# Optimization experiments

Hardware: AMD Instinct MI355X
Metric: run time of the kernel (lower is better)

Reference implementation:

```python
import jax, jax.numpy as jnp
import numpy as np

BS, C_IN, H, W = 16, 128, 64, 64
C_OUT, K, STRIDE, PAD, DIL = 256, 3, 1, 1, 1
ALPHA = 0.5  # scaling_factor
QMAX = 127.0  # int8 symmetric fake-quant


def _fake_quant(t):
    # symmetric per-tensor int8 fake quantization with straight-through estimator
    s = jax.lax.stop_gradient(jnp.max(jnp.abs(t))) / QMAX
    s = jnp.where(s == 0, 1.0, s)
    q = jnp.clip(jnp.round(t / s), -QMAX, QMAX) * s
    return t + jax.lax.stop_gradient(q - t)  # STE


def setup_inputs() -> dict:
    key = jax.random.key(0)
    k1, k2, k3 = jax.random.split(key, 3)
    x = jax.random.normal(k1, (BS, C_IN, H, W), dtype=jnp.float32)
    weight = jax.random.normal(k2, (C_OUT, C_IN, K, K), dtype=jnp.float32) * 0.05
    bias = jax.random.normal(k3, (C_OUT,), dtype=jnp.float32) * 0.01
    return {"x": x, "weight": weight, "bias": bias}


def reference(x, weight, bias):
    bs, _, h_in, w_in = x.shape
    ickhkw = C_IN * K * K
    h_out = (h_in + 2 * PAD - DIL * (K - 1) - 1) // STRIDE + 1
    w_out = (w_in + 2 * PAD - DIL * (K - 1) - 1) // STRIDE + 1

    # im2col (matches torch F.unfold feature ordering: channel-major, then kh, kw)
    patches = jax.lax.conv_general_dilated_patches(
        x, filter_shape=(K, K), window_strides=(STRIDE, STRIDE),
        padding=((PAD, PAD), (PAD, PAD)), rhs_dilation=(DIL, DIL),
    )  # [bs, ickhkw, h_out, w_out]
    cols = patches.reshape(bs, ickhkw, h_out * w_out)
    cols = cols.transpose(0, 2, 1).reshape(-1, ickhkw)  # [bs*L, ickhkw]

    w2 = weight.reshape(C_OUT, ickhkw)

    # SmoothQuant per-column scales (detached)
    w_scale = jax.lax.stop_gradient(jnp.max(jnp.abs(w2), axis=0))    # [ickhkw]
    act_scale = jax.lax.stop_gradient(jnp.max(jnp.abs(cols), axis=0))  # [ickhkw]
    scale = act_scale ** ALPHA / w_scale ** (1.0 - ALPHA)
    scale = jnp.where(scale == 0, 1.0, scale)

    w_s = _fake_quant(w2 * scale)
    x_s = _fake_quant(cols / scale)

    out = x_s @ w_s.T  # [bs*L, C_OUT]
    out = out.reshape(bs, h_out * w_out, C_OUT).transpose(0, 2, 1)
    out = out.reshape(bs, C_OUT, h_out, w_out)
    return out + bias.reshape(1, C_OUT, 1, 1)
```

## Files before the change

### kernel.cpp

```cpp
#include <hip/hip_runtime.h>
#include <cstdint>

#define C_IN   128
#define C_OUT  256
#define KK     1152
#define NPIX   4096
#define BS     16
#define M_ROWS 65536
#define QMAXF  127.0f

typedef int v4i __attribute__((ext_vector_type(4)));

#define OFF_QW    75497472
#define OFF_SCALE 75792384
#define OFF_QMUL  75796992
#define OFF_APART 75801600
#define OFF_SCAL  75843072

__global__ void k_prep(const float* __restrict__ x, const float* __restrict__ wgt,
                       float* __restrict__ act_part, float* __restrict__ w_part) {
    const int tid = threadIdx.x;
    if (blockIdx.x >= 1024) {
        int t = blockIdx.x - 1024;
        int j = (t % 5) * 256 + tid;
        int s = t / 5;
        if (j >= KK) return;
        const float* p = wgt + (size_t)s * 16 * KK + j;
        float m = 0.f;
#pragma unroll
        for (int i = 0; i < 16; i++) m = fmaxf(m, fabsf(p[(size_t)i * KK]));
        w_part[s * KK + j] = m;
        return;
    }
    const int c = blockIdx.x >> 3, s = blockIdx.x & 7;
    float m[9];
#pragma unroll
    for (int i = 0; i < 9; i++) m[i] = 0.f;
    for (int p = tid; p < 2 * NPIX; p += 256) {
        int b = s * 2 + (p >> 12);
        int hw = p & 4095;
        int h = hw >> 6, w = hw & 63;
        float v = fabsf(x[b * (C_IN * NPIX) + c * NPIX + hw]);
        bool rr[3] = { h <= 62, true, h >= 1 };
        bool cc[3] = { w <= 62, true, w >= 1 };
#pragma unroll
        for (int i = 0; i < 3; i++)
#pragma unroll
            for (int jq = 0; jq < 3; jq++)
                m[i * 3 + jq] = fmaxf(m[i * 3 + jq], (rr[i] && cc[jq]) ? v : 0.f);
    }
    __shared__ float sm[9][4];
    int lane = tid & 63, wid = tid >> 6;
#pragma unroll
    for (int i = 0; i < 9; i++) {
        float v = m[i];
        for (int off = 32; off > 0; off >>= 1) v = fmaxf(v, __shfl_down(v, off));
        if (lane == 0) sm[i][wid] = v;
    }
    __syncthreads();
    if (tid < 9) {
        float v = fmaxf(fmaxf(sm[tid][0], sm[tid][1]), fmaxf(sm[tid][2], sm[tid][3]));
        act_part[s * KK + c * 9 + tid] = v;
    }
}

__global__ void k_scales(const float* __restrict__ act_part, const float* __restrict__ w_part,
                         float* __restrict__ scale, float* __restrict__ qmul,
                         float* __restrict__ scalars) {
    const int tid = threadIdx.x;
    float sc_local[2] = {1.f, 1.f};
    float mx = 0.f, mw = 0.f;
#pragma unroll
    for (int t = 0; t < 2; t++) {
        int j = tid + t * 1024;
        if (j < KK) {
            float a = 0.f;
#pragma unroll
            for (int s = 0; s < 8; s++) a = fmaxf(a, act_part[s * KK + j]);
            float wv = 0.f;
#pragma unroll
            for (int s = 0; s < 16; s++) wv = fmaxf(wv, w_part[s * KK + j]);
            float sc = sqrtf(a) / sqrtf(wv);
            if (sc == 0.f) sc = 1.0f;
            scale[j] = sc;
            sc_local[t] = sc;
            mx = fmaxf(mx, a / sc);
            mw = fmaxf(mw, wv * sc);
        }
    }
    __shared__ float smx[16], smw[16];
    __shared__ float s_x_sh;
    int lane = tid & 63, wid = tid >> 6;
    for (int off = 32; off > 0; off >>= 1) {
        mx = fmaxf(mx, __shfl_down(mx, off));
        mw = fmaxf(mw, __shfl_down(mw, off));
    }
    if (lane == 0) { smx[wid] = mx; smw[wid] = mw; }
    __syncthreads();
    if (tid == 0) {
        float a = 0.f, b = 0.f;
        for (int i = 0; i < 16; i++) { a = fmaxf(a, smx[i]); b = fmaxf(b, smw[i]); }
        float s_x = a / QMAXF; if (s_x == 0.f) s_x = 1.f;
        float s_w = b / QMAXF; if (s_w == 0.f) s_w = 1.f;
        scalars[0] = s_x; scalars[1] = s_w; scalars[2] = s_x * s_w;
        s_x_sh = s_x;
    }
    __syncthreads();
    float s_x = s_x_sh;
#pragma unroll
    for (int t = 0; t < 2; t++) {
        int j = tid + t * 1024;
        if (j < KK) qmul[j] = 1.0f / (sc_local[t] * s_x);
    }
}

__global__ void k_quant_w(const float* __restrict__ wgt, const float* __restrict__ scale,
                          const float* __restrict__ scalars, signed char* __restrict__ qWp) {
    int idx = blockIdx.x * 256 + threadIdx.x;
    int m  = (unsigned)idx / KK;
    int kp = idx - m * KK;
    int tap = kp >> 7, c = kp & 127;
    int j = c * 9 + tap;
    float s_w = scalars[1];
    float t = wgt[m * KK + j] * scale[j];
    float q = rintf(t / s_w);
    q = fminf(fmaxf(q, -QMAXF), QMAXF);
    qWp[idx] = (signed char)(int)q;
}

#define PRODUCE(TP, XV, BSP)                                                    \
    do {                                                                        \
        const int g_ = (TP) / 3, jj_ = (TP) - g_ * 3, sh_ = jj_ - 1;            \
        const bool rowok_ = ((unsigned)(oh - 1 + g_)) < 64u;                    \
        int n_ = lane - sh_;                                                    \
        bool valid_ = (unsigned)n_ < 64u;                                       \
        int wrow_ = valid_ ? n_ : (sh_ == -1 ? 0 : 63);                         \
        bool live_ = rowok_ && valid_;                                          \
        const float* qmt_ = qm + (TP) * 128 + c0;                               \
        int pk_[4];                                                             \
        _Pragma("unroll")                                                       \
        for (int d4 = 0; d4 < 4; d4++) {                                        \
            int w_ = 0;                                                         \
            _Pragma("unroll")                                                   \
            for (int e = 0; e < 4; e++) {                                       \
                float v_ = live_ ? XV[d4 * 4 + e] : 0.f;                        \
                float q_ = rintf(v_ * qmt_[d4 * 4 + e]);                        \
                q_ = fminf(fmaxf(q_, -QMAXF), QMAXF);                           \
                w_ |= ((int)q_ & 255) << (8 * e);                               \
            }                                                                   \
            pk_[d4] = w_;                                                       \
        }                                                                       \
        *(v4i*)((BSP) + wrow_ * 128 + ((wv ^ (wrow_ & 7)) * 16)) =              \
            (v4i){pk_[0], pk_[1], pk_[2], pk_[3]};                              \
    } while (0)

__global__ __launch_bounds__(512, 4) void k_gemm(const signed char* __restrict__ qWp,
                                                 const float* __restrict__ x,
                                                 const float* __restrict__ qmul,
                                                 const float* __restrict__ scalars,
                                                 const float* __restrict__ bias,
                                                 float* __restrict__ out) {
    __shared__ __align__(16) signed char Bs[2][64 * 128];
    __shared__ float qm[KK];
    const int tid = threadIdx.x;
    const int lane = tid & 63, wv = tid >> 6;
    const int b  = blockIdx.x >> 6;
    const int oh = blockIdx.x & 63;
    const float* xb = x + (size_t)b * (C_IN * NPIX);
    const int c0 = wv * 16;

    for (int i = tid; i < KK; i += 512) {
        int tap = i >> 7, c = i & 127;
        qm[i] = qmul[c * 9 + tap];
    }

    const signed char* aBase = qWp + (size_t)(wv * 32 + (lane & 15)) * KK + (lane >> 4) * 16;

    v4i acc[2][4];
#pragma unroll
    for (int i = 0; i < 2; i++)
#pragma unroll
        for (int jq = 0; jq < 4; jq++) acc[i][jq] = (v4i){0, 0, 0, 0};

    float xr[16], xrn[16];
    {
        const bool ok = oh >= 1;
        const float* s = xb + (oh - 1) * 64 + lane;
#pragma unroll
        for (int d = 0; d < 16; d++) xr[d] = ok ? s[(size_t)(c0 + d) * NPIX] : 0.f;
    }
    v4i af[2][2], afn[2][2];
#pragma unroll
    for (int h = 0; h < 2; h++)
#pragma unroll
        for (int mt = 0; mt < 2; mt++)
            af[h][mt] = *(const v4i*)(aBase + (size_t)mt * 16 * KK + 0 * 128 + h * 64);

    __syncthreads();

    PRODUCE(0, xr, (signed char*)Bs[0]);

    {
        const float* sp = xb + oh * 64 + lane;
#pragma unroll
        for (int d = 0; d < 16; d++) xrn[d] = sp[(size_t)(c0 + d) * NPIX];
    }

    __syncthreads();

#pragma unroll
    for (int t = 0; t < 9; t++) {
        const signed char* bsR = (const signed char*)Bs[t & 1];
        signed char* bsW = (signed char*)Bs[(t + 1) & 1];

        v4i bf0[4];
#pragma unroll
        for (int nt = 0; nt < 4; nt++) {
            int rb = nt * 16 + (lane & 15);
            int q4 = (lane >> 4);
            bf0[nt] = *(const v4i*)(bsR + rb * 128 + ((q4 ^ (rb & 7)) * 16));
        }

        if (t < 8) {
#pragma unroll
            for (int h = 0; h < 2; h++)
#pragma unroll
                for (int mt = 0; mt < 2; mt++)
                    afn[h][mt] = *(const v4i*)(aBase + (size_t)mt * 16 * KK + (t + 1) * 128 + h * 64);
        }

        if (t == 2) {
            const bool ok = (oh + 1) < 64;
            const float* sp = xb + (oh + 1) * 64 + lane;
#pragma unroll
            for (int d = 0; d < 16; d++) xr[d] = ok ? sp[(size_t)(c0 + d) * NPIX] : 0.f;
        }

        if (t < 8) {
            const int tap = t + 1;
            const int g = tap / 3;
            if (g == 1) PRODUCE(tap, xrn, bsW);
            else        PRODUCE(tap, xr,  bsW);
        }

#pragma unroll
        for (int mt = 0; mt < 2; mt++)
#pragma unroll
            for (int nt = 0; nt < 4; nt++)
                acc[mt][nt] = __builtin_amdgcn_mfma_i32_16x16x64_i8(af[0][mt], bf0[nt], acc[mt][nt], 0, 0, 0);

        v4i bf1[4];
#pragma unroll
        for (int nt = 0; nt < 4; nt++) {
            int rb = nt * 16 + (lane & 15);
            int q4 = 4 + (lane >> 4);
            bf1[nt] = *(const v4i*)(bsR + rb * 128 + ((q4 ^ (rb & 7)) * 16));
        }
#pragma unroll
        for (int mt = 0; mt < 2; mt++)
#pragma unroll
            for (int nt = 0; nt < 4; nt++)
                acc[mt][nt] = __builtin_amdgcn_mfma_i32_16x16x64_i8(af[1][mt], bf1[nt], acc[mt][nt], 0, 0, 0);

        if (t < 8) {
#pragma unroll
            for (int h = 0; h < 2; h++)
#pragma unroll
                for (int mt = 0; mt < 2; mt++) af[h][mt] = afn[h][mt];
            __syncthreads();
        }
    }

    const float ssp = scalars[2];
    const int quad = lane >> 4, col = lane & 15;
    float bv[2][4];
#pragma unroll
    for (int mt = 0; mt < 2; mt++)
#pragma unroll
        for (int rg = 0; rg < 4; rg++)
            bv[mt][rg] = bias[wv * 32 + mt * 16 + quad * 4 + rg];

    float* obase = out + ((size_t)b * C_OUT) * NPIX + oh * 64;
#pragma unroll
    for (int mt = 0; mt < 2; mt++) {
#pragma unroll
        for (int nt = 0; nt < 4; nt++) {
            int n = nt * 16 + col;
#pragma unroll
            for (int rg = 0; rg < 4; rg++) {
                int m = wv * 32 + mt * 16 + quad * 4 + rg;
                obase[(size_t)m * NPIX + n] = (float)acc[mt][nt][rg] * ssp + bv[mt][rg];
            }
        }
    }
}

extern "C" void kernel_launch(void* const* d_in, const int* in_sizes, int n_in,
                              void* d_out, int out_size, void* d_ws, size_t ws_size,
                              hipStream_t stream) {
    const float* x    = (const float*)d_in[0];
    const float* wgt  = (const float*)d_in[1];
    const float* bias = (const float*)d_in[2];
    float* out = (float*)d_out;

    char* ws = (char*)d_ws;
    signed char* qWp = (signed char*)(ws + OFF_QW);
    float* w_part    = (float*)(ws + OFF_QW);
    float* scale     = (float*)(ws + OFF_SCALE);
    float* qmul      = (float*)(ws + OFF_QMUL);
    float* act_part  = (float*)(ws + OFF_APART);
    float* scalars   = (float*)(ws + OFF_SCAL);

    k_prep<<<1104, 256, 0, stream>>>(x, wgt, act_part, w_part);
    k_scales<<<1, 1024, 0, stream>>>(act_part, w_part, scale, qmul, scalars);
    k_quant_w<<<(C_OUT * KK) / 256, 256, 0, stream>>>(wgt, scale, scalars, qWp);
    k_gemm<<<BS * 64, 512, 0, stream>>>(qWp, x, qmul, scalars, bias, out);
}
```

Baseline: 171.9 us.

## Batch three taps per LDS stage and streamline int8 packing in conv GEMM

The per-tap double-buffered loop is replaced by stages that each produce three taps (one input row) into a larger shared buffer. This cuts block barriers from nine to three and lets MFMA work on one row overlap the quantisation of the next. Quantisation packing now uses byte-permute instructions instead of clamp, shift and or, relying on the scales keeping values inside the int8 range and on out-of-range rows already being zero. Blocks are also remapped for better cache locality. The tripled LDS footprint may reduce how many blocks fit per CU.

New measurement: 156.4 us. 9.0% less time.

```diff
diff --git a/kernel.cpp b/kernel.cpp
--- a/kernel.cpp
+++ b/kernel.cpp
@@ -130,28 +130,59 @@
 
 #define PRODUCE(TP, XV, BSP)                                                    \
     do {                                                                        \
-        const int g_ = (TP) / 3, jj_ = (TP) - g_ * 3, sh_ = jj_ - 1;            \
-        const bool rowok_ = ((unsigned)(oh - 1 + g_)) < 64u;                    \
+        const int jj_ = (TP) % 3, sh_ = jj_ - 1;                                \
         int n_ = lane - sh_;                                                    \
         bool valid_ = (unsigned)n_ < 64u;                                       \
         int wrow_ = valid_ ? n_ : (sh_ == -1 ? 0 : 63);                         \
-        bool live_ = rowok_ && valid_;                                          \
         const float* qmt_ = qm + (TP) * 128 + c0;                               \
         int pk_[4];                                                             \
         _Pragma("unroll")                                                       \
         for (int d4 = 0; d4 < 4; d4++) {                                        \
-            int w_ = 0;                                                         \
-            _Pragma("unroll")                                                   \
-            for (int e = 0; e < 4; e++) {                                       \
-                float v_ = live_ ? XV[d4 * 4 + e] : 0.f;                        \
-                float q_ = rintf(v_ * qmt_[d4 * 4 + e]);                        \
-                q_ = fminf(fmaxf(q_, -QMAXF), QMAXF);                           \
-                w_ |= ((int)q_ & 255) << (8 * e);                               \
-            }                                                                   \
-            pk_[d4] = w_;                                                       \
+            int q0_ = (int)rintf(XV[d4 * 4 + 0] * qmt_[d4 * 4 + 0]);            \
+            int q1_ = (int)rintf(XV[d4 * 4 + 1] * qmt_[d4 * 4 + 1]);            \
+            int q2_ = (int)rintf(XV[d4 * 4 + 2] * qmt_[d4 * 4 + 2]);            \
+            int q3_ = (int)rintf(XV[d4 * 4 + 3] * qmt_[d4 * 4 + 3]);            \
+            unsigned t0_ = __builtin_amdgcn_perm((unsigned)q1_, (unsigned)q0_, 0x0c0c0400u); \
+            unsigned t1_ = __builtin_amdgcn_perm((unsigned)q3_, (unsigned)q2_, 0x0c0c0400u); \
+            int w_ = (int)__builtin_amdgcn_perm(t1_, t0_, 0x05040100u);         \
+            pk_[d4] = valid_ ? w_ : 0;                                          \
         }                                                                       \
         *(v4i*)((BSP) + wrow_ * 128 + ((wv ^ (wrow_ & 7)) * 16)) =              \
             (v4i){pk_[0], pk_[1], pk_[2], pk_[3]};                              \
+    } while (0)
+
+#define MFMA_TAP(TP, BSP)                                                       \
+    do {                                                                        \
+        if ((TP) < 8) {                                                         \
+            _Pragma("unroll")                                                   \
+            for (int h = 0; h < 2; h++)                                         \
+                _Pragma("unroll")                                               \
+                for (int mt = 0; mt < 2; mt++)                                  \
+                    afn[h][mt] = *(const v4i*)(aBase + (size_t)mt * 16 * KK +   \
+                                               ((TP) + 1) * 128 + h * 64);      \
+        }                                                                       \
+        _Pragma("unroll")                                                       \
+        for (int h = 0; h < 2; h++) {                                           \
+            const int q4_ = h * 4 + (lane >> 4);                                \
+            v4i bf_[4];                                                         \
+            _Pragma("unroll")                                                   \
+            for (int nt = 0; nt < 4; nt++) {                                    \
+                int rb_ = nt * 16 + (lane & 15);                                \
+                bf_[nt] = *(const v4i*)((BSP) + rb_ * 128 + ((q4_ ^ (rb_ & 7)) * 16)); \
+            }                                                                   \
+            _Pragma("unroll")                                                   \
+            for (int mt = 0; mt < 2; mt++)                                      \
+                _Pragma("unroll")                                               \
+                for (int nt = 0; nt < 4; nt++)                                  \
+                    acc[mt][nt] = __builtin_amdgcn_mfma_i32_16x16x64_i8(        \
+                        af[h][mt], bf_[nt], acc[mt][nt], 0, 0, 0);              \
+        }                                                                       \
+        if ((TP) < 8) {                                                         \
+            _Pragma("unroll")                                                   \
+            for (int h = 0; h < 2; h++)                                         \
+                _Pragma("unroll")                                               \
+                for (int mt = 0; mt < 2; mt++) af[h][mt] = afn[h][mt];          \
+        }                                                                       \
     } while (0)
 
 __global__ __launch_bounds__(512, 4) void k_gemm(const signed char* __restrict__ qWp,
@@ -160,12 +191,14 @@
                                                  const float* __restrict__ scalars,
                                                  const float* __restrict__ bias,
                                                  float* __restrict__ out) {
-    __shared__ __align__(16) signed char Bs[2][64 * 128];
+    __shared__ __align__(16) signed char Bs[2][3][64 * 128];
     __shared__ float qm[KK];
     const int tid = threadIdx.x;
     const int lane = tid & 63, wv = tid >> 6;
-    const int b  = blockIdx.x >> 6;
-    const int oh = blockIdx.x & 63;
+    const int bid = blockIdx.x;
+    const int swz = (bid & 7) * 128 + (bid >> 3);
+    const int b  = swz >> 6;
+    const int oh = swz & 63;
     const float* xb = x + (size_t)b * (C_IN * NPIX);
     const int c0 = wv * 16;
 
@@ -189,6 +222,11 @@
 #pragma unroll
         for (int d = 0; d < 16; d++) xr[d] = ok ? s[(size_t)(c0 + d) * NPIX] : 0.f;
     }
+    {
+        const float* sp = xb + oh * 64 + lane;
+#pragma unroll
+        for (int d = 0; d < 16; d++) xrn[d] = sp[(size_t)(c0 + d) * NPIX];
+    }
     v4i af[2][2], afn[2][2];
 #pragma unroll
     for (int h = 0; h < 2; h++)
@@ -198,78 +236,38 @@
 
     __syncthreads();
 
-    PRODUCE(0, xr, (signed char*)Bs[0]);
+    PRODUCE(0, xr, (signed char*)Bs[0][0]);
+    PRODUCE(1, xr, (signed char*)Bs[0][1]);
+    PRODUCE(2, xr, (signed char*)Bs[0][2]);
 
     {
-        const float* sp = xb + oh * 64 + lane;
-#pragma unroll
-        for (int d = 0; d < 16; d++) xrn[d] = sp[(size_t)(c0 + d) * NPIX];
-    }
-
-    __syncthreads();
-
-#pragma unroll
-    for (int t = 0; t < 9; t++) {
-        const signed char* bsR = (const signed char*)Bs[t & 1];
-        signed char* bsW = (signed char*)Bs[(t + 1) & 1];
-
-        v4i bf0[4];
-#pragma unroll
-        for (int nt = 0; nt < 4; nt++) {
-            int rb = nt * 16 + (lane & 15);
-            int q4 = (lane >> 4);
-            bf0[nt] = *(const v4i*)(bsR + rb * 128 + ((q4 ^ (rb & 7)) * 16));
-        }
-
-        if (t < 8) {
-#pragma unroll
-            for (int h = 0; h < 2; h++)
-#pragma unroll
-                for (int mt = 0; mt < 2; mt++)
-                    afn[h][mt] = *(const v4i*)(aBase + (size_t)mt * 16 * KK + (t + 1) * 128 + h * 64);
-        }
-
-        if (t == 2) {
-            const bool ok = (oh + 1) < 64;
-            const float* sp = xb + (oh + 1) * 64 + lane;
-#pragma unroll
-            for (int d = 0; d < 16; d++) xr[d] = ok ? sp[(size_t)(c0 + d) * NPIX] : 0.f;
-        }
-
-        if (t < 8) {
-            const int tap = t + 1;
-            const int g = tap / 3;
-            if (g == 1) PRODUCE(tap, xrn, bsW);
-            else        PRODUCE(tap, xr,  bsW);
-        }
-
-#pragma unroll
-        for (int mt = 0; mt < 2; mt++)
-#pragma unroll
-            for (int nt = 0; nt < 4; nt++)
-                acc[mt][nt] = __builtin_amdgcn_mfma_i32_16x16x64_i8(af[0][mt], bf0[nt], acc[mt][nt], 0, 0, 0);
-
-        v4i bf1[4];
-#pragma unroll
-        for (int nt = 0; nt < 4; nt++) {
-            int rb = nt * 16 + (lane & 15);
-            int q4 = 4 + (lane >> 4);
-            bf1[nt] = *(const v4i*)(bsR + rb * 128 + ((q4 ^ (rb & 7)) * 16));
-        }
-#pragma unroll
-        for (int mt = 0; mt < 2; mt++)
-#pragma unroll
-            for (int nt = 0; nt < 4; nt++)
-                acc[mt][nt] = __builtin_amdgcn_mfma_i32_16x16x64_i8(af[1][mt], bf1[nt], acc[mt][nt], 0, 0, 0);
-
-        if (t < 8) {
-#pragma unroll
-            for (int h = 0; h < 2; h++)
-#pragma unroll
-                for (int mt = 0; mt < 2; mt++) af[h][mt] = afn[h][mt];
-            __syncthreads();
-        }
-    }
+        const bool ok = (oh + 1) < 64;
+        const float* sp = xb + (oh + 1) * 64 + lane;
+#pragma unroll
+        for (int d = 0; d < 16; d++) xr[d] = ok ? sp[(size_t)(c0 + d) * NPIX] : 0.f;
+    }
+
+    __syncthreads();
+
+    PRODUCE(3, xrn, (signed char*)Bs[1][0]);
+    PRODUCE(4, xrn, (signed char*)Bs[1][1]);
+    PRODUCE(5, xrn, (signed char*)Bs[1][2]);
+    MFMA_TAP(0, (const signed char*)Bs[0][0]);
+    MFMA_TAP(1, (const signed char*)Bs[0][1]);
+    MFMA_TAP(2, (const signed char*)Bs[0][2]);
+    __syncthreads();
+
+    PRODUCE(6, xr, (signed char*)Bs[0][0]);
+    PRODUCE(7, xr, (signed char*)Bs[0][1]);
+    PRODUCE(8, xr, (signed char*)Bs[0][2]);
+    MFMA_TAP(3, (const signed char*)Bs[1][0]);
+    MFMA_TAP(4, (const signed char*)Bs[1][1]);
+    MFMA_TAP(5, (const signed char*)Bs[1][2]);
+    __syncthreads();
+
+    MFMA_TAP(6, (const signed char*)Bs[0][0]);
+    MFMA_TAP(7, (const signed char*)Bs[0][1]);
+    MFMA_TAP(8, (const signed char*)Bs[0][2]);
 
     const float ssp = scalars[2];
     const int quad = lane >> 4, col = lane & 15;
```
